# Optimization experiments

Hardware: AMD Instinct MI355X
Metric: run time of the kernel (lower is better)

Reference implementation:

```python
import jax, jax.numpy as jnp
import numpy as np

N_NODES = 100000
N_EDGES = 3200000
N_GRAPHS = 4096
BN_EPS = 1e-5


def setup_inputs() -> dict:
    key = jax.random.key(0)
    ks = iter(jax.random.split(key, 64))
    d = {}
    d["x"] = jax.random.normal(next(ks), (N_NODES, 36), dtype=jnp.float32)
    d["edge_index"] = jax.random.randint(next(ks), (2, N_EDGES), 0, N_NODES, dtype=jnp.int32)
    d["batch"] = jnp.sort(jax.random.randint(next(ks), (N_NODES,), 0, N_GRAPHS, dtype=jnp.int32))
    d["num_graphs"] = N_GRAPHS
    # GCN layers: (in, out) per hidden_dims=[128,128,64]
    dims = [(36, 128), (128, 128), (128, 64)]
    for i, (di, do) in enumerate(dims):
        d[f"w{i}"] = jax.random.normal(next(ks), (di, do), dtype=jnp.float32) * (1.0 / np.sqrt(di))
        d[f"b{i}"] = jax.random.normal(next(ks), (do,), dtype=jnp.float32) * 0.01
        d[f"g{i}"] = jax.random.uniform(next(ks), (do,), dtype=jnp.float32, minval=0.5, maxval=1.5)
        d[f"be{i}"] = jax.random.normal(next(ks), (do,), dtype=jnp.float32) * 0.01
        d[f"m{i}"] = jax.random.normal(next(ks), (do,), dtype=jnp.float32) * 0.01
        d[f"v{i}"] = jax.random.uniform(next(ks), (do,), dtype=jnp.float32, minval=0.5, maxval=1.5)
    # FC head: 64 -> 128 -> 64 -> 2
    d["fw0"] = jax.random.normal(next(ks), (64, 128), dtype=jnp.float32) * (1.0 / 8.0)
    d["fb0"] = jax.random.normal(next(ks), (128,), dtype=jnp.float32) * 0.01
    d["fw1"] = jax.random.normal(next(ks), (128, 64), dtype=jnp.float32) * (1.0 / np.sqrt(128))
    d["fb1"] = jax.random.normal(next(ks), (64,), dtype=jnp.float32) * 0.01
    d["ow"] = jax.random.normal(next(ks), (64, 2), dtype=jnp.float32) * (1.0 / 8.0)
    d["ob"] = jax.random.normal(next(ks), (2,), dtype=jnp.float32) * 0.01
    return d


def _gcn_layer(x, w, b, src, dst, norm_e, norm_self, n_nodes):
    # PyG GCNConv with self-loops: out[i] = sum_j norm_ij * (x_j @ W) + b
    xw = x @ w                                   # [N, out]
    msg = xw[src] * norm_e[:, None]              # gather + scale, [E, out]
    agg = jax.ops.segment_sum(msg, dst, num_segments=n_nodes)
    return agg + xw * norm_self[:, None] + b     # self-loop contribution + bias


def _bn_eval(x, g, be, m, v):
    return g * (x - m) * jax.lax.rsqrt(v + BN_EPS) + be


def reference(x, edge_index, batch, num_graphs,
              w0, b0, g0, be0, m0, v0,
              w1, b1, g1, be1, m1, v1,
              w2, b2, g2, be2, m2, v2,
              fw0, fb0, fw1, fb1, ow, ob):
    n = x.shape[0]
    src, dst = edge_index[0], edge_index[1]
    # symmetric GCN normalization with self-loops (gcn_norm)
    deg = jax.ops.segment_sum(jnp.ones(src.shape[0], x.dtype), dst, num_segments=n) + 1.0
    dinv = jax.lax.rsqrt(deg)
    norm_e = dinv[src] * dinv[dst]   # per-edge coeff
    norm_self = dinv * dinv          # self-loop coeff = 1/deg

    params = [(w0, b0, g0, be0, m0, v0), (w1, b1, g1, be1, m1, v1), (w2, b2, g2, be2, m2, v2)]
    h = x
    for (w, b, g, be, m, v) in params:
        h = _gcn_layer(h, w, b, src, dst, norm_e, norm_self, n)
        h = jax.nn.relu(_bn_eval(h, g, be, m, v))  # dropout inactive in eval

    # global mean pool over graphs
    sums = jax.ops.segment_sum(h, batch, num_segments=num_graphs)          # [G, 64]
    cnt = jax.ops.segment_sum(jnp.ones(n, h.dtype), batch, num_segments=num_graphs)
    pooled = sums / jnp.maximum(cnt, 1.0)[:, None]

    h = jax.nn.relu(pooled @ fw0 + fb0)
    h = jax.nn.relu(h @ fw1 + fb1)
    return h @ ow + ob
```

## Files before the change

### kernel.cpp

```cpp
#include <hip/hip_runtime.h>
#include <hip/hip_fp16.h>

#define BN_EPS 1e-5f

#define BUCK_SHIFT 9
#define NBUCK_MAX 256
#define BCAP 20480
#define PBLK 512

typedef _Float16 f16x8 __attribute__((ext_vector_type(8)));
typedef float f32x4 __attribute__((ext_vector_type(4)));

__global__ __launch_bounds__(256) void prep0(const float* __restrict__ w0,
                                             const float* __restrict__ w1,
                                             const float* __restrict__ w2,
                                             __half* __restrict__ Wp0,
                                             __half* __restrict__ Wp1,
                                             __half* __restrict__ Wp2,
                                             int* __restrict__ gcnt,
                                             float* __restrict__ pool,
                                             float* __restrict__ cnt, int G) {
    const int tid = threadIdx.x;
    if (blockIdx.x == 0) {
        for (int idx = tid; idx < 8 * 4 * 64 * 8; idx += 256) {
            int j = idx & 7, lane = (idx >> 3) & 63, kb = (idx >> 9) & 3, nt = idx >> 11;
            int k = kb * 32 + (lane >> 4) * 8 + j, c = nt * 16 + (lane & 15);
            Wp1[idx] = __float2half_rn(w1[k * 128 + c]);
        }
    } else if (blockIdx.x == 1) {
        for (int idx = tid; idx < 4 * 4 * 64 * 8; idx += 256) {
            int j = idx & 7, lane = (idx >> 3) & 63, kb = (idx >> 9) & 3, nt = idx >> 11;
            int k = kb * 32 + (lane >> 4) * 8 + j, c = nt * 16 + (lane & 15);
            Wp2[idx] = __float2half_rn(w2[k * 64 + c]);
        }
    } else if (blockIdx.x == 2) {
        for (int idx = tid; idx < 8 * 2 * 64 * 8; idx += 256) {
            int j = idx & 7, lane = (idx >> 3) & 63, kb = (idx >> 9) & 1, nt = idx >> 10;
            int k = kb * 32 + (lane >> 4) * 8 + j, c = nt * 16 + (lane & 15);
            Wp0[idx] = (k < 36) ? __float2half_rn(w0[k * 128 + c]) : __float2half_rn(0.0f);
        }
    } else {
        const int zb = blockIdx.x - 3;
        const int nzb = gridDim.x - 3;
        const int tot = G * 64 + G + 256;
        for (int i = zb * 256 + tid; i < tot; i += nzb * 256) {
            if (i < G * 64) pool[i] = 0.0f;
            else if (i < G * 64 + G) cnt[i - G * 64] = 0.0f;
            else gcnt[i - G * 64 - G] = 0;
        }
    }
}

__global__ __launch_bounds__(256) void fused_scatter(const int* __restrict__ src,
                                                     const int* __restrict__ dst,
                                                     int* __restrict__ gcnt,
                                                     int* __restrict__ ebuf,
                                                     int nE, int nbuck, int chunk) {
    __shared__ int h[NBUCK_MAX], rbase[NBUCK_MAX], cur[NBUCK_MAX];
    const int blk = blockIdx.x, tid = threadIdx.x;
    for (int j = tid; j < nbuck; j += 256) { h[j] = 0; cur[j] = 0; }
    __syncthreads();
    const int base = blk * chunk;
    const int end = min(base + chunk, nE);
    for (int i = base + tid; i < end; i += 256)
        atomicAdd(&h[dst[i] >> BUCK_SHIFT], 1);
    __syncthreads();
    for (int j = tid; j < nbuck; j += 256)
        rbase[j] = h[j] ? atomicAdd(&gcnt[j], h[j]) : 0;
    __syncthreads();
    for (int i = base + tid; i < end; i += 256) {
        int s = src[i], d = dst[i];
        int b = d >> BUCK_SHIFT;
        int p = rbase[b] + atomicAdd(&cur[b], 1);
        if (p < BCAP) ebuf[(size_t)b * BCAP + p] = ((d & 511) << 17) | s;
    }
}

__global__ __launch_bounds__(256) void fused_csr(const int* __restrict__ ebuf,
                                                 const int* __restrict__ gcnt,
                                                 const float* __restrict__ x,
                                                 const int* __restrict__ batch,
                                                 int* __restrict__ degI,
                                                 float* __restrict__ dinv,
                                                 int* __restrict__ row_start,
                                                 int* __restrict__ src_sorted,
                                                 __half* __restrict__ xs_h,
                                                 float* __restrict__ cnt, int n) {
    __shared__ int deg[512];
    __shared__ int cur[512];
    __shared__ float sdi[512];
    __shared__ int tmp[256];
    __shared__ int s_low_total;
    const int b = blockIdx.x, tid = threadIdx.x;
    const int nb = b << BUCK_SHIFT;
    const int cntb = min(gcnt[b], BCAP);
    const int* __restrict__ eb = ebuf + (size_t)b * BCAP;

    for (int j = tid; j < 512; j += 256) deg[j] = 0;
    __syncthreads();
    for (int i = tid; i < cntb; i += 256)
        atomicAdd(&deg[((unsigned)eb[i]) >> 17], 1);
    __syncthreads();

    for (int j = tid; j < 512; j += 256) {
        int node = nb + j;
        if (node < n) {
            int d = deg[j];
            degI[node] = d;
            float di = rsqrtf((float)d + 1.0f);
            dinv[node] = di;
            sdi[j] = di;
        }
    }

    int v0 = deg[tid];
    tmp[tid] = v0;
    __syncthreads();
    for (int off = 1; off < 256; off <<= 1) {
        int t = (tid >= off) ? tmp[tid - off] : 0;
        __syncthreads();
        tmp[tid] += t;
        __syncthreads();
    }
    int ex_low = tmp[tid] - v0;
    if (tid == 255) s_low_total = tmp[255];
    __syncthreads();
    int low_total = s_low_total;
    int v1 = deg[256 + tid];
    __syncthreads();
    tmp[tid] = v1;
    __syncthreads();
    for (int off = 1; off < 256; off <<= 1) {
        int t = (tid >= off) ? tmp[tid - off] : 0;
        __syncthreads();
        tmp[tid] += t;
        __syncthreads();
    }
    int ex_high = tmp[tid] - v1 + low_total;

    const int gbase = b * BCAP;
    if (nb + tid < n) row_start[nb + tid] = gbase + ex_low;
    if (nb + 256 + tid < n) row_start[nb + 256 + tid] = gbase + ex_high;
    cur[tid] = ex_low;
    cur[256 + tid] = ex_high;
    __syncthreads();

    for (int i = tid; i < cntb; i += 256) {
        unsigned ed = (unsigned)eb[i];
        int p = atomicAdd(&cur[ed >> 17], 1);
        src_sorted[gbase + p] = (int)(ed & 0x1FFFFu);
    }

    for (int idx = tid; idx < 512 * 18; idx += 256) {
        int j = idx / 18;
        int node = nb + j;
        if (node < n) {
            int c = idx - j * 18;
            float2 v = *(const float2*)(x + (size_t)node * 36 + 2 * c);
            float di = sdi[j];
            *(__half2*)(xs_h + (size_t)node * 36 + 2 * c) = __floats2half2_rn(v.x * di, v.y * di);
        }
    }

    for (int j = tid; j < 512; j += 256) {
        int node = nb + j;
        if (node < n) unsafeAtomicAdd(&cnt[batch[node]], 1.0f);
    }
}

template<int LDK, int KB, int OUT, int NT, bool BNRELU, bool SCALEOUT>
__global__ __launch_bounds__(256) void gemm_mfma(const __half* __restrict__ in,
                                                 const __half* __restrict__ Wp,
                                                 const float* __restrict__ bias,
                                                 const float* __restrict__ gg,
                                                 const float* __restrict__ bb,
                                                 const float* __restrict__ mm,
                                                 const float* __restrict__ vv,
                                                 const float* __restrict__ dscale,
                                                 __half* __restrict__ out, int n) {
    const int lane = threadIdx.x & 63;
    const int wave = threadIdx.x >> 6;
    const int r0 = blockIdx.x * 64 + wave * 16;
    const int arow = r0 + (lane & 15);
    const int kg = lane >> 4;

    f16x8 a[KB];
#pragma unroll
    for (int kb = 0; kb < KB; kb++)
        a[kb] = *(const f16x8*)(in + (size_t)arow * LDK + kb * 32 + kg * 8);

    f32x4 acc[NT];
#pragma unroll
    for (int nt = 0; nt < NT; nt++) {
        f32x4 z = {0.0f, 0.0f, 0.0f, 0.0f};
        acc[nt] = z;
    }

#pragma unroll
    for (int nt = 0; nt < NT; nt++) {
#pragma unroll
        for (int kb = 0; kb < KB; kb++) {
            f16x8 b = *(const f16x8*)(Wp + ((size_t)(nt * KB + kb) * 64 + lane) * 8);
            acc[nt] = __builtin_amdgcn_mfma_f32_16x16x32_f16(a[kb], b, acc[nt], 0, 0, 0);
        }
    }

    const int col = lane & 15;
    const int rbase = r0 + kg * 4;
    float ds[4] = {1.f, 1.f, 1.f, 1.f};
    if constexpr (SCALEOUT) {
#pragma unroll
        for (int r = 0; r < 4; r++) ds[r] = dscale[rbase + r];
    }
#pragma unroll
    for (int nt = 0; nt < NT; nt++) {
        const int c = nt * 16 + col;
        float s = 1.f, t = 0.f;
        if constexpr (BNRELU) {
            s = gg[c] * rsqrtf(vv[c] + BN_EPS);
            t = bb[c] + (bias[c] - mm[c]) * s;
        }
#pragma unroll
        for (int r = 0; r < 4; r++) {
            float val = acc[nt][r];
            if constexpr (BNRELU) val = fmaxf(val * s + t, 0.0f);
            if constexpr (SCALEOUT) val *= ds[r];
            out[(size_t)(rbase + r) * OUT + c] = __float2half_rn(val);
        }
    }
}

__global__ __launch_bounds__(256) void gemm12_mfma(const __half* __restrict__ in,
                                                   const __half* __restrict__ Wp1,
                                                   const float* __restrict__ b1,
                                                   const float* __restrict__ g1,
                                                   const float* __restrict__ be1,
                                                   const float* __restrict__ m1,
                                                   const float* __restrict__ v1,
                                                   const __half* __restrict__ Wp2,
                                                   const float* __restrict__ dscale,
                                                   __half* __restrict__ out, int n) {
    __shared__ __align__(16) _Float16 s_h[4][16][136];
    const int lane = threadIdx.x & 63;
    const int wave = threadIdx.x >> 6;
    const int r0 = blockIdx.x * 64 + wave * 16;
    const int arow = r0 + (lane & 15);
    const int kg = lane >> 4;
    const int col = lane & 15;

    f16x8 a[4];
#pragma unroll
    for (int kb = 0; kb < 4; kb++)
        a[kb] = *(const f16x8*)(in + (size_t)arow * 128 + kb * 32 + kg * 8);

    f32x4 acc1[8];
#pragma unroll
    for (int nt = 0; nt < 8; nt++) {
        f32x4 z = {0.0f, 0.0f, 0.0f, 0.0f};
        acc1[nt] = z;
    }
#pragma unroll
    for (int nt = 0; nt < 8; nt++) {
#pragma unroll
        for (int kb = 0; kb < 4; kb++) {
            f16x8 b = *(const f16x8*)(Wp1 + ((size_t)(nt * 4 + kb) * 64 + lane) * 8);
            acc1[nt] = __builtin_amdgcn_mfma_f32_16x16x32_f16(a[kb], b, acc1[nt], 0, 0, 0);
        }
    }

#pragma unroll
    for (int nt = 0; nt < 8; nt++) {
        const int c = nt * 16 + col;
        float s = g1[c] * rsqrtf(v1[c] + BN_EPS);
        float t = be1[c] + (b1[c] - m1[c]) * s;
#pragma unroll
        for (int r = 0; r < 4; r++) {
            float val = fmaxf(acc1[nt][r] * s + t, 0.0f);
            s_h[wave][kg * 4 + r][c] = (_Float16)val;
        }
    }

    f16x8 a2[4];
#pragma unroll
    for (int kb = 0; kb < 4; kb++)
        a2[kb] = *(const f16x8*)&s_h[wave][col][kb * 32 + kg * 8];

    f32x4 acc2[4];
#pragma unroll
    for (int nt = 0; nt < 4; nt++) {
        f32x4 z = {0.0f, 0.0f, 0.0f, 0.0f};
        acc2[nt] = z;
    }
#pragma unroll
    for (int nt = 0; nt < 4; nt++) {
#pragma unroll
        for (int kb = 0; kb < 4; kb++) {
            f16x8 b = *(const f16x8*)(Wp2 + ((size_t)(nt * 4 + kb) * 64 + lane) * 8);
            acc2[nt] = __builtin_amdgcn_mfma_f32_16x16x32_f16(a2[kb], b, acc2[nt], 0, 0, 0);
        }
    }

    const int rbase = r0 + kg * 4;
    float ds[4];
#pragma unroll
    for (int r = 0; r < 4; r++) ds[r] = dscale[rbase + r];
#pragma unroll
    for (int nt = 0; nt < 4; nt++) {
        const int c = nt * 16 + col;
#pragma unroll
        for (int r = 0; r < 4; r++)
            out[(size_t)(rbase + r) * 64 + c] = __float2half_rn(acc2[nt][r] * ds[r]);
    }
}

__global__ __launch_bounds__(256) void agg_pull36w_h(const __half* __restrict__ xs_h,
                                                     const int* __restrict__ row_start,
                                                     const int* __restrict__ degI,
                                                     const int* __restrict__ src_sorted,
                                                     const float* __restrict__ dinv,
                                                     __half* __restrict__ out, int n) {
    int node = __builtin_amdgcn_readfirstlane((int)(blockIdx.x * 4 + (threadIdx.x >> 6)));
    if (node >= n) return;
    const int lane = threadIdx.x & 63;
    int e = row_start[node];
    const int re = e + degI[node];
    const float di = dinv[node];

    const char* __restrict__ xb = (const char*)xs_h;
    const unsigned loff = (unsigned)lane << 2;

    float2 acc = make_float2(0.f, 0.f);
    if (lane < 18) acc = __half22float2(*(const __half2*)(xb + ((unsigned)node * 72u + loff)));

    for (; e + 3 < re; e += 4) {
        int s0 = src_sorted[e], s1 = src_sorted[e + 1],
            s2 = src_sorted[e + 2], s3 = src_sorted[e + 3];
        if (lane < 18) {
            float2 a0 = __half22float2(*(const __half2*)(xb + ((unsigned)s0 * 72u + loff)));
            float2 a1 = __half22float2(*(const __half2*)(xb + ((unsigned)s1 * 72u + loff)));
            float2 a2 = __half22float2(*(const __half2*)(xb + ((unsigned)s2 * 72u + loff)));
            float2 a3 = __half22float2(*(const __half2*)(xb + ((unsigned)s3 * 72u + loff)));
            acc.x += (a0.x + a1.x) + (a2.x + a3.x);
            acc.y += (a0.y + a1.y) + (a2.y + a3.y);
        }
    }
    for (; e < re; e++) {
        int s = src_sorted[e];
        if (lane < 18) {
            float2 a = __half22float2(*(const __half2*)(xb + ((unsigned)s * 72u + loff)));
            acc.x += a.x;
            acc.y += a.y;
        }
    }
    if (lane < 32) {
        __half2 o = __floats2half2_rn(acc.x * di, acc.y * di);
        *(__half2*)((char*)out + (((unsigned)node << 7) + loff)) = o;
    }
}

__global__ __launch_bounds__(256) void agg_pull_wave2_h(const __half* __restrict__ feat_h,
                                                        const int* __restrict__ row_start,
                                                        const int* __restrict__ degI,
                                                        const int* __restrict__ src_sorted,
                                                        const float* __restrict__ dinv,
                                                        __half* __restrict__ out, int n) {
    int node = __builtin_amdgcn_readfirstlane((int)(blockIdx.x * 4 + (threadIdx.x >> 6)));
    if (node >= n) return;
    const int lane = threadIdx.x & 63;
    int e = row_start[node];
    const int re = e + degI[node];
    const float di = dinv[node];

    const char* __restrict__ fb = (const char*)feat_h;
    const unsigned loff = (unsigned)lane << 2;

    float2 acc = __half22float2(*(const __half2*)(fb + (((unsigned)node << 8) + loff)));

    for (; e + 3 < re; e += 4) {
        int s0 = src_sorted[e], s1 = src_sorted[e + 1],
            s2 = src_sorted[e + 2], s3 = src_sorted[e + 3];
        float2 a0 = __half22float2(*(const __half2*)(fb + (((unsigned)s0 << 8) + loff)));
        float2 a1 = __half22float2(*(const __half2*)(fb + (((unsigned)s1 << 8) + loff)));
        float2 a2 = __half22float2(*(const __half2*)(fb + (((unsigned)s2 << 8) + loff)));
        float2 a3 = __half22float2(*(const __half2*)(fb + (((unsigned)s3 << 8) + loff)));
        acc.x += (a0.x + a1.x) + (a2.x + a3.x);
        acc.y += (a0.y + a1.y) + (a2.y + a3.y);
    }
    for (; e < re; e++) {
        int s = src_sorted[e];
        float2 a = __half22float2(*(const __half2*)(fb + (((unsigned)s << 8) + loff)));
        acc.x += a.x;
        acc.y += a.y;
    }
    __half2 o = __floats2half2_rn(acc.x * di, acc.y * di);
    *(__half2*)((char*)out + (((unsigned)node << 8) + loff)) = o;
}

__global__ __launch_bounds__(256) void agg_pull_pool_h(const __half* __restrict__ feat_h,
                                                       const int* __restrict__ row_start,
                                                       const int* __restrict__ degI,
                                                       const int* __restrict__ src_sorted,
                                                       const float* __restrict__ dinv,
                                                       const float* __restrict__ bias,
                                                       const float* __restrict__ gg,
                                                       const float* __restrict__ bb,
                                                       const float* __restrict__ mm,
                                                       const float* __restrict__ vv,
                                                       const int* __restrict__ batch,
                                                       float* __restrict__ pool, int n) {
    int node = __builtin_amdgcn_readfirstlane((int)(blockIdx.x * 4 + (threadIdx.x >> 6)));
    if (node >= n) return;
    const int lane = threadIdx.x & 63;
    int e = row_start[node];
    const int re = e + degI[node];
    const float di = dinv[node];

    const char* __restrict__ fb = (const char*)feat_h;
    const unsigned loff = (unsigned)lane << 1;

    float acc = __half2float(*(const __half*)(fb + (((unsigned)node << 7) + loff)));

    for (; e + 3 < re; e += 4) {
        int s0 = src_sorted[e], s1 = src_sorted[e + 1],
            s2 = src_sorted[e + 2], s3 = src_sorted[e + 3];
        float a0 = __half2float(*(const __half*)(fb + (((unsigned)s0 << 7) + loff)));
        float a1 = __half2float(*(const __half*)(fb + (((unsigned)s1 << 7) + loff)));
        float a2 = __half2float(*(const __half*)(fb + (((unsigned)s2 << 7) + loff)));
        float a3 = __half2float(*(const __half*)(fb + (((unsigned)s3 << 7) + loff)));
        acc += (a0 + a1) + (a2 + a3);
    }
    for (; e < re; e++) {
        acc += __half2float(*(const __half*)(fb + (((unsigned)src_sorted[e] << 7) + loff)));
    }
    float h = acc * di + bias[lane];
    float scale = gg[lane] * rsqrtf(vv[lane] + BN_EPS);
    float val = fmaxf((h - mm[lane]) * scale + bb[lane], 0.0f);
    unsafeAtomicAdd(&pool[(size_t)batch[node] * 64 + lane], val);
}

__global__ __launch_bounds__(128) void fc_head_kernel(const float* __restrict__ pool,
                                                      const float* __restrict__ cnt,
                                                      const float* __restrict__ fw0,
                                                      const float* __restrict__ fb0,
                                                      const float* __restrict__ fw1,
                                                      const float* __restrict__ fb1,
                                                      const float* __restrict__ ow,
                                                      const float* __restrict__ ob,
                                                      float* __restrict__ out) {
    int g = blockIdx.x, tid = threadIdx.x;
    __shared__ float p[64], h1[128], h2[64];
    if (tid < 64) p[tid] = pool[g * 64 + tid] / fmaxf(cnt[g], 1.0f);
    __syncthreads();
    {
        float acc = fb0[tid];
        for (int k = 0; k < 64; k++) acc += p[k] * fw0[k * 128 + tid];
        h1[tid] = fmaxf(acc, 0.0f);
    }
    __syncthreads();
    if (tid < 64) {
        float acc = fb1[tid];
        for (int k = 0; k < 128; k++) acc += h1[k] * fw1[k * 64 + tid];
        h2[tid] = fmaxf(acc, 0.0f);
    }
    __syncthreads();
    if (tid < 2) {
        float acc = ob[tid];
        for (int k = 0; k < 64; k++) acc += h2[k] * ow[k * 2 + tid];
        out[g * 2 + tid] = acc;
    }
}

extern "C" void kernel_launch(void* const* d_in, const int* in_sizes, int n_in,
                              void* d_out, int out_size, void* d_ws, size_t ws_size,
                              hipStream_t stream) {
    const float* x     = (const float*)d_in[0];
    const int*   eidx  = (const int*)d_in[1];
    const int*   batch = (const int*)d_in[2];
    const float* w0 = (const float*)d_in[4];
    const float* b0 = (const float*)d_in[5];
    const float* g0 = (const float*)d_in[6];
    const float* be0 = (const float*)d_in[7];
    const float* m0 = (const float*)d_in[8];
    const float* v0 = (const float*)d_in[9];
    const float* w1 = (const float*)d_in[10];
    const float* b1 = (const float*)d_in[11];
    const float* g1 = (const float*)d_in[12];
    const float* be1 = (const float*)d_in[13];
    const float* m1 = (const float*)d_in[14];
    const float* v1 = (const float*)d_in[15];
    const float* w2 = (const float*)d_in[16];
    const float* b2 = (const float*)d_in[17];
    const float* g2 = (const float*)d_in[18];
    const float* be2 = (const float*)d_in[19];
    const float* m2 = (const float*)d_in[20];
    const float* v2 = (const float*)d_in[21];
    const float* fw0 = (const float*)d_in[22];
    const float* fb0 = (const float*)d_in[23];
    const float* fw1 = (const float*)d_in[24];
    const float* fb1 = (const float*)d_in[25];
    const float* ow = (const float*)d_in[26];
    const float* ob = (const float*)d_in[27];

    const int N = in_sizes[0] / 36;
    const int E = in_sizes[1] / 2;
    const int G = out_size / 2;
    const int* src = eidx;
    const int* dst = eidx + E;

    const int nbuck = (N + 511) >> BUCK_SHIFT;
    const int chunk = (E + PBLK - 1) / PBLK;
    const int NPAD = ((N + 63) / 64) * 64;
    const int NGP = NPAD / 64;

    char* wsb = (char*)d_ws;
    int*    ebuf       = (int*)wsb;     wsb += (size_t)nbuck * BCAP * 4;
    __half* F1         = (__half*)wsb;  wsb += (size_t)NPAD * 128 * 2;
    __half* F1a        = (__half*)wsb;  wsb += (size_t)NPAD * 128 * 2;
    __half* F2         = (__half*)wsb;  wsb += (size_t)NPAD * 64 * 2;
    __half* A36h       = (__half*)wsb;  wsb += (size_t)NPAD * 64 * 2;
    __half* xs_h       = (__half*)wsb;  wsb += (size_t)N * 36 * 2;
    int*    src_sorted = (int*)wsb;     wsb += (size_t)nbuck * BCAP * 4;
    int*    degI       = (int*)wsb;     wsb += (size_t)N * 4;
    int*    row_start  = (int*)wsb;     wsb += (size_t)N * 4;
    float*  dinv       = (float*)wsb;   wsb += (size_t)NPAD * 4;
    float*  pool       = (float*)wsb;   wsb += (size_t)G * 64 * 4;
    float*  cnt        = (float*)wsb;   wsb += (size_t)G * 4;
    int*    gcnt       = (int*)wsb;     wsb += 256 * 4;
    __half* Wp0        = (__half*)wsb;  wsb += 8192 * 2;
    __half* Wp1        = (__half*)wsb;  wsb += 16384 * 2;
    __half* Wp2        = (__half*)wsb;  wsb += 8192 * 2;

    prep0<<<64, 256, 0, stream>>>(w0, w1, w2, Wp0, Wp1, Wp2, gcnt, pool, cnt, G);

    fused_scatter<<<PBLK, 256, 0, stream>>>(src, dst, gcnt, ebuf, E, nbuck, chunk);
    fused_csr<<<nbuck, 256, 0, stream>>>(ebuf, gcnt, x, batch, degI, dinv, row_start,
                                         src_sorted, xs_h, cnt, N);

    const int NW = (N + 3) / 4;

    agg_pull36w_h<<<NW, 256, 0, stream>>>(xs_h, row_start, degI, src_sorted, dinv, A36h, N);
    gemm_mfma<64, 2, 128, 8, true, true><<<NGP, 256, 0, stream>>>(
        A36h, Wp0, b0, g0, be0, m0, v0, dinv, F1, N);

    agg_pull_wave2_h<<<NW, 256, 0, stream>>>(F1, row_start, degI, src_sorted, dinv, F1a, N);
    gemm12_mfma<<<NGP, 256, 0, stream>>>(F1a, Wp1, b1, g1, be1, m1, v1, Wp2, dinv, F2, N);

    agg_pull_pool_h<<<NW, 256, 0, stream>>>(
        F2, row_start, degI, src_sorted, dinv, b2, g2, be2, m2, v2, batch, pool, N);

    fc_head_kernel<<<G, 128, 0, stream>>>(pool, cnt, fw0, fb0, fw1, fb1, ow, ob, (float*)d_out);
}
```

Before: 552.5 us.

## Store layer-1 features in column slices and aggregate per slice for cache locality

The first GEMM now writes its 128-wide output as eight 16-column slices, each laid out contiguously across all nodes. A new aggregation kernel handles one slice per block, so each gather touches a 3.2 MB slice that fits in L2 instead of the full 25 MB feature matrix. Inside a wave, 8 edge groups of 8 lanes each read 32-byte rows, and a shuffle reduction combines them. In exchange, each gather is small (32 B per edge) and the edge list is read eight times, and each wave walks 128 nodes in sequence.

```diff
diff --git a/kernel.cpp b/kernel.cpp
--- a/kernel.cpp
+++ b/kernel.cpp
@@ -168,7 +168,7 @@
     }
 }
 
-template<int LDK, int KB, int OUT, int NT, bool BNRELU, bool SCALEOUT>
+template<int LDK, int KB, int OUT, int NT, bool BNRELU, bool SCALEOUT, bool OUTSLICE>
 __global__ __launch_bounds__(256) void gemm_mfma(const __half* __restrict__ in,
                                                  const __half* __restrict__ Wp,
                                                  const float* __restrict__ bias,
@@ -177,7 +177,7 @@
                                                  const float* __restrict__ mm,
                                                  const float* __restrict__ vv,
                                                  const float* __restrict__ dscale,
-                                                 __half* __restrict__ out, int n) {
+                                                 __half* __restrict__ out, int n, int npad) {
     const int lane = threadIdx.x & 63;
     const int wave = threadIdx.x >> 6;
     const int r0 = blockIdx.x * 64 + wave * 16;
@@ -225,7 +225,60 @@
             float val = acc[nt][r];
             if constexpr (BNRELU) val = fmaxf(val * s + t, 0.0f);
             if constexpr (SCALEOUT) val *= ds[r];
-            out[(size_t)(rbase + r) * OUT + c] = __float2half_rn(val);
+            if constexpr (OUTSLICE)
+                out[(size_t)nt * npad * 16 + (size_t)(rbase + r) * 16 + col] = __float2half_rn(val);
+            else
+                out[(size_t)(rbase + r) * OUT + c] = __float2half_rn(val);
+        }
+    }
+}
+
+__global__ __launch_bounds__(256) void agg_pull_slice(const __half* __restrict__ Ts,
+                                                      const int* __restrict__ row_start,
+                                                      const int* __restrict__ degI,
+                                                      const int* __restrict__ src_sorted,
+                                                      const float* __restrict__ dinv,
+                                                      __half* __restrict__ out,
+                                                      int n, int npad) {
+    const int slice = blockIdx.x & 7;
+    const int chunk = blockIdx.x >> 3;
+    const int wave = threadIdx.x >> 6;
+    const int lane = threadIdx.x & 63;
+    const int eg = lane >> 3;
+    const int cp = lane & 7;
+    const __half* __restrict__ T = Ts + (size_t)slice * npad * 16;
+    const int n0 = chunk * 512 + wave * 128;
+
+    for (int i = 0; i < 128; i++) {
+        const int node = n0 + i;
+        if (node >= n) break;
+        int e = row_start[node];
+        const int re = e + degI[node];
+        const float di = dinv[node];
+        float2 acc = make_float2(0.f, 0.f);
+        if (eg == 0) {
+            acc = __half22float2(*(const __half2*)(T + (size_t)node * 16 + cp * 2));
+        }
+        for (; e + 8 <= re; e += 8) {
+            int s = src_sorted[e + eg];
+            float2 a = __half22float2(*(const __half2*)(T + (size_t)s * 16 + cp * 2));
+            acc.x += a.x;
+            acc.y += a.y;
+        }
+        if (e + eg < re) {
+            int s = src_sorted[e + eg];
+            float2 a = __half22float2(*(const __half2*)(T + (size_t)s * 16 + cp * 2));
+            acc.x += a.x;
+            acc.y += a.y;
+        }
+#pragma unroll
+        for (int off = 8; off < 64; off <<= 1) {
+            acc.x += __shfl_xor(acc.x, off);
+            acc.y += __shfl_xor(acc.y, off);
+        }
+        if (eg == 0) {
+            __half2 o = __floats2half2_rn(acc.x * di, acc.y * di);
+            *(__half2*)(out + (size_t)node * 128 + slice * 16 + cp * 2) = o;
         }
     }
 }
@@ -356,44 +409,6 @@
         __half2 o = __floats2half2_rn(acc.x * di, acc.y * di);
         *(__half2*)((char*)out + (((unsigned)node << 7) + loff)) = o;
     }
-}
-
-__global__ __launch_bounds__(256) void agg_pull_wave2_h(const __half* __restrict__ feat_h,
-                                                        const int* __restrict__ row_start,
-                                                        const int* __restrict__ degI,
-                                                        const int* __restrict__ src_sorted,
-                                                        const float* __restrict__ dinv,
-                                                        __half* __restrict__ out, int n) {
-    int node = __builtin_amdgcn_readfirstlane((int)(blockIdx.x * 4 + (threadIdx.x >> 6)));
-    if (node >= n) return;
-    const int lane = threadIdx.x & 63;
-    int e = row_start[node];
-    const int re = e + degI[node];
-    const float di = dinv[node];
-
-    const char* __restrict__ fb = (const char*)feat_h;
-    const unsigned loff = (unsigned)lane << 2;
-
-    float2 acc = __half22float2(*(const __half2*)(fb + (((unsigned)node << 8) + loff)));
-
-    for (; e + 3 < re; e += 4) {
-        int s0 = src_sorted[e], s1 = src_sorted[e + 1],
-            s2 = src_sorted[e + 2], s3 = src_sorted[e + 3];
-        float2 a0 = __half22float2(*(const __half2*)(fb + (((unsigned)s0 << 8) + loff)));
-        float2 a1 = __half22float2(*(const __half2*)(fb + (((unsigned)s1 << 8) + loff)));
-        float2 a2 = __half22float2(*(const __half2*)(fb + (((unsigned)s2 << 8) + loff)));
-        float2 a3 = __half22float2(*(const __half2*)(fb + (((unsigned)s3 << 8) + loff)));
-        acc.x += (a0.x + a1.x) + (a2.x + a3.x);
-        acc.y += (a0.y + a1.y) + (a2.y + a3.y);
-    }
-    for (; e < re; e++) {
-        int s = src_sorted[e];
-        float2 a = __half22float2(*(const __half2*)(fb + (((unsigned)s << 8) + loff)));
-        acc.x += a.x;
-        acc.y += a.y;
-    }
-    __half2 o = __floats2half2_rn(acc.x * di, acc.y * di);
-    *(__half2*)((char*)out + (((unsigned)node << 8) + loff)) = o;
 }
 
 __global__ __launch_bounds__(256) void agg_pull_pool_h(const __half* __restrict__ feat_h,
@@ -514,7 +529,7 @@
 
     char* wsb = (char*)d_ws;
     int*    ebuf       = (int*)wsb;     wsb += (size_t)nbuck * BCAP * 4;
-    __half* F1         = (__half*)wsb;  wsb += (size_t)NPAD * 128 * 2;
+    __half* F1s        = (__half*)wsb;  wsb += (size_t)NPAD * 128 * 2;
     __half* F1a        = (__half*)wsb;  wsb += (size_t)NPAD * 128 * 2;
     __half* F2         = (__half*)wsb;  wsb += (size_t)NPAD * 64 * 2;
     __half* A36h       = (__half*)wsb;  wsb += (size_t)NPAD * 64 * 2;
@@ -539,10 +554,14 @@
     const int NW = (N + 3) / 4;
 
     agg_pull36w_h<<<NW, 256, 0, stream>>>(xs_h, row_start, degI, src_sorted, dinv, A36h, N);
-    gemm_mfma<64, 2, 128, 8, true, true><<<NGP, 256, 0, stream>>>(
-        A36h, Wp0, b0, g0, be0, m0, v0, dinv, F1, N);
-
-    agg_pull_wave2_h<<<NW, 256, 0, stream>>>(F1, row_start, degI, src_sorted, dinv, F1a, N);
+    gemm_mfma<64, 2, 128, 8, true, true, true><<<NGP, 256, 0, stream>>>(
+        A36h, Wp0, b0, g0, be0, m0, v0, dinv, F1s, N, NPAD);
+
+    {
+        const int nchunk = (N + 511) / 512;
+        agg_pull_slice<<<nchunk * 8, 256, 0, stream>>>(
+            F1s, row_start, degI, src_sorted, dinv, F1a, N, NPAD);
+    }
     gemm12_mfma<<<NGP, 256, 0, stream>>>(F1a, Wp1, b1, g1, be1, m1, v1, Wp2, dinv, F2, N);
 
     agg_pull_pool_h<<<NW, 256, 0, stream>>>(
```

Result: slower. 837.1 us (+51.5%).
